# Performance work log

Measured on AMD Instinct MI355X. Metric: run time of the kernel, lower is better.

## Reference

```python
import jax, jax.numpy as jnp
import numpy as np

NEG_SLOPE = 0.01  # torch F.leaky_relu default


def _leaky_relu(v):
    return jnp.where(v >= 0, v, NEG_SLOPE * v)


def _att_layer(t, w1, w2):
    # t: [b, c, n] ; SE-style channel attention with scalar gate
    y = t.mean(axis=-1)                                   # [b, c] (AdaptiveAvgPool1d(1))
    y = jax.nn.sigmoid(jax.nn.relu(y @ w1.T) @ w2.T)       # [b, 1]
    return t * y[:, :, None]


def _avwgcn(x, node_emb, supports, cheb, wpool, bpool, iw, ib, gw, gb,
            a1w1, a1w2, a2w1, a2w2):
    # x: [b, n, c_in]; supports/cheb: [k, n, n]
    b, n, _ = x.shape
    weights = jnp.einsum('nd,dkio->nkio', node_emb, wpool)   # per-node dyn weights
    bias = node_emb @ bpool                                  # [n, o]
    x_g = jnp.einsum('knm,bmc->bnkc', supports, x)           # [b, n, k, c_in]
    x_gconv0 = jnp.einsum('bnki,nkio->bno', x_g, weights) + bias
    x0 = x @ iw.T + ib                                       # init_gconv: [b, n, o]
    x_g1 = jnp.einsum('knm,bmc->bnkc', cheb, x0).reshape(b, n, -1)
    x_gconv1 = x_g1 @ gw.T + gb                              # [b, n, o]
    out = (_att_layer(_leaky_relu(x_gconv0).transpose(0, 2, 1), a1w1, a1w2)
           + _att_layer(_leaky_relu(x_gconv1).transpose(0, 2, 1), a2w1, a2w2))
    return out.transpose(0, 2, 1)                            # [b, n, o]


def _cheb_supports(L, k):
    n = L.shape[0]
    s = [jnp.eye(n, dtype=L.dtype), L]
    for _ in range(2, k):
        s.append(2.0 * L @ s[-1] - s[-2])
    return jnp.stack(s, axis=0)  # [k, n, n]


B, N, DIN, DOUT, K, ED = 64, 1024, 32, 64, 3, 16
CIN = DIN + DOUT  # 96 (gate/update input = cat(x, state))


def setup_inputs() -> dict:
    key = jax.random.key(0)
    ks = jax.random.split(key, 32)
    g = lambda i, shape, s=0.1: jax.random.normal(ks[i], shape, dtype=jnp.float32) * s
    inp = {
        'x': jax.random.normal(ks[0], (B, N, DIN), dtype=jnp.float32),
        'state': jax.random.normal(ks[1], (B, N, DOUT), dtype=jnp.float32),
        'node_embeddings': jax.random.normal(ks[2], (N, ED), dtype=jnp.float32),
        'learned_tilde': jax.random.normal(ks[3], (N, N), dtype=jnp.float32) / np.sqrt(N),
        'cheb_polynomials': jax.random.normal(ks[4], (K, N, N), dtype=jnp.float32) / np.sqrt(N),
        # gate AVWGCN: dim_in=96, dim_out=2*DOUT=128
        'gate_wpool': g(5, (ED, K, CIN, 2 * DOUT)),
        'gate_bpool': g(6, (ED, 2 * DOUT)),
        'gate_iw': g(7, (2 * DOUT, CIN)), 'gate_ib': g(8, (2 * DOUT,)),
        'gate_gw': g(9, (2 * DOUT, 2 * DOUT * K)), 'gate_gb': g(10, (2 * DOUT,)),
        'gate_a1w1': g(11, (2 * DOUT // 16, 2 * DOUT)), 'gate_a1w2': g(12, (1, 2 * DOUT // 16)),
        'gate_a2w1': g(13, (2 * DOUT // 16, 2 * DOUT)), 'gate_a2w2': g(14, (1, 2 * DOUT // 16)),
        # update AVWGCN: dim_in=96, dim_out=DOUT=64
        'upd_wpool': g(15, (ED, K, CIN, DOUT)),
        'upd_bpool': g(16, (ED, DOUT)),
        'upd_iw': g(17, (DOUT, CIN)), 'upd_ib': g(18, (DOUT,)),
        'upd_gw': g(19, (DOUT, DOUT * K)), 'upd_gb': g(20, (DOUT,)),
        'upd_a1w1': g(21, (DOUT // 16, DOUT)), 'upd_a1w2': g(22, (1, DOUT // 16)),
        'upd_a2w1': g(23, (DOUT // 16, DOUT)), 'upd_a2w2': g(24, (1, DOUT // 16)),
    }
    return inp


def reference(x, state, node_embeddings, learned_tilde, cheb_polynomials,
              gate_wpool, gate_bpool, gate_iw, gate_ib, gate_gw, gate_gb,
              gate_a1w1, gate_a1w2, gate_a2w1, gate_a2w2,
              upd_wpool, upd_bpool, upd_iw, upd_ib, upd_gw, upd_gb,
              upd_a1w1, upd_a1w2, upd_a2w1, upd_a2w2):
    supports = _cheb_supports(learned_tilde, K)  # [k, n, n]
    inp_state = jnp.concatenate([x, state], axis=-1)  # [b, n, din+dout]
    z_r = jax.nn.sigmoid(_avwgcn(inp_state, node_embeddings, supports, cheb_polynomials,
                                 gate_wpool, gate_bpool, gate_iw, gate_ib, gate_gw, gate_gb,
                                 gate_a1w1, gate_a1w2, gate_a2w1, gate_a2w2))
    z, r = jnp.split(z_r, 2, axis=-1)
    candidate = jnp.concatenate([x, z * state], axis=-1)
    hc = jnp.tanh(_avwgcn(candidate, node_embeddings, supports, cheb_polynomials,
                          upd_wpool, upd_bpool, upd_iw, upd_ib, upd_gw, upd_gb,
                          upd_a1w1, upd_a1w2, upd_a2w1, upd_a2w2))
    h = r * state + (1.0 - r) * hc
    return h
```

## Files before the change

### kernel.cpp

```cpp
#include <hip/hip_runtime.h>
#include <hip/hip_bf16.h>
#include <math.h>


#define B_  64
#define N_  1024
#define CIN_ 96
#define R_  288

typedef __attribute__((ext_vector_type(8))) short bf16x8;
typedef __attribute__((ext_vector_type(4))) float f32x4;
typedef unsigned short u16;
typedef unsigned int u32;

__device__ __forceinline__ float lrelu(float v) { return v >= 0.f ? v : 0.01f * v; }
__device__ __forceinline__ float sigmoidf_(float u) { return 1.f / (1.f + expf(-u)); }
__device__ __forceinline__ u16 f2b(float f) {
  union { float f; u32 u; } c; c.f = f;
  u32 u = c.u;
  return (u16)((u + 0x7FFFu + ((u >> 16) & 1u)) >> 16);
}
__device__ __forceinline__ float b2f(u16 u) {
  union { u32 x; float f; } c; c.x = ((u32)u) << 16; return c.f;
}
__device__ __forceinline__ void gload_lds16(const u16* gp, u16* lp) {
  __builtin_amdgcn_global_load_lds((const __attribute__((address_space(1))) u32*)gp,
                                   (__attribute__((address_space(3))) u32*)lp, 16, 0, 0);
}

__global__ __launch_bounds__(256) void concat_bf2(const float* __restrict__ x,
                                                  const float* __restrict__ st,
                                                  float* __restrict__ inp,
                                                  u16* __restrict__ inpb) {
  size_t t = (size_t)blockIdx.x * 256 + threadIdx.x;
  if (t >= (size_t)B_ * N_ * CIN_) return;
  int i = (int)(t % CIN_);
  size_t v = t / CIN_;
  size_t b = v & 63, n = v >> 6;
  float f = (i < 32) ? x[(b * N_ + n) * 32 + i] : st[(b * N_ + n) * 64 + (i - 32)];
  inp[t] = f;
  inpb[t] = f2b(f);
}

__global__ __launch_bounds__(256) void conv_f2b(const float* __restrict__ in,
                                                u16* __restrict__ out, int n4) {
  int t = blockIdx.x * 256 + threadIdx.x;
  if (t >= n4) return;
  float4 v = ((const float4*)in)[t];
  ushort4 o;
  o.x = f2b(v.x); o.y = f2b(v.y); o.z = f2b(v.z); o.w = f2b(v.w);
  ((ushort4*)out)[t] = o;
}

__global__ __launch_bounds__(256) void split_hilo(const float* __restrict__ in,
                                                  u16* __restrict__ hi,
                                                  u16* __restrict__ lo, int n4) {
  int t = blockIdx.x * 256 + threadIdx.x;
  if (t >= n4) return;
  float4 v = ((const float4*)in)[t];
  ushort4 h, l;
  h.x = f2b(v.x); l.x = f2b(v.x - b2f(h.x));
  h.y = f2b(v.y); l.y = f2b(v.y - b2f(h.y));
  h.z = f2b(v.z); l.z = f2b(v.z - b2f(h.z));
  h.w = f2b(v.w); l.w = f2b(v.w - b2f(h.w));
  ((ushort4*)hi)[t] = h;
  ((ushort4*)lo)[t] = l;
}

__global__ __launch_bounds__(256) void transpose_split(const float* __restrict__ in,
                                                       u16* __restrict__ hiT,
                                                       u16* __restrict__ loT) {
  __shared__ float t[32][33];
  const int tid = threadIdx.x;
  const int j0 = blockIdx.x * 32, r0 = blockIdx.y * 32;
  const int tc = tid & 31, tr = tid >> 5;
#pragma unroll
  for (int q = 0; q < 4; ++q)
    t[tr + q * 8][tc] = in[(size_t)(r0 + tr + q * 8) * 1024 + j0 + tc];
  __syncthreads();
  const int jj = tid >> 3, rq = (tid & 7) * 4;
  ushort4 h, l;
#pragma unroll
  for (int q = 0; q < 4; ++q) {
    float v = t[rq + q][jj];
    u16 hh = f2b(v);
    ((u16*)&h)[q] = hh;
    ((u16*)&l)[q] = f2b(v - b2f(hh));
  }
  *(ushort4*)(hiT + (size_t)(j0 + jj) * N_ + r0 + rq) = h;
  *(ushort4*)(loT + (size_t)(j0 + jj) * N_ + r0 + rq) = l;
}

__global__ __launch_bounds__(256) void transpose_b2b(const u16* __restrict__ Z, int Zs,
                                                     int Ctot, u16* __restrict__ Zt) {
  __shared__ u16 t[32][36];
  const int tid = threadIdx.x;
  const int c0 = blockIdx.x * 32, n0 = blockIdx.y * 32, b = blockIdx.z;
  {
    const int i = tid >> 3, c4 = (tid & 7) * 4;
    ushort4 v = *(const ushort4*)(Z + ((size_t)(n0 + i) * 64 + b) * Zs + c0 + c4);
    t[i][c4] = v.x; t[i][c4 + 1] = v.y; t[i][c4 + 2] = v.z; t[i][c4 + 3] = v.w;
  }
  __syncthreads();
  {
    const int c = tid >> 3, n4 = (tid & 7) * 4;
    ushort4 o;
    o.x = t[n4][c]; o.y = t[n4 + 1][c]; o.z = t[n4 + 2][c]; o.w = t[n4 + 3][c];
    *(ushort4*)(Zt + (size_t)(b * Ctot + c0 + c) * 1024 + n0 + n4) = o;
  }
}

__global__ __launch_bounds__(256) void mfma_l2p(const u16* __restrict__ Lhi,
                                                const u16* __restrict__ Llo,
                                                const u16* __restrict__ LhiT,
                                                const u16* __restrict__ LloT,
                                                float* __restrict__ P) {
  __shared__ u16 Asl[64 * 64];
  __shared__ u16 Bsl[64 * 64];
  const int tid = threadIdx.x;
  const int w = tid >> 6, lane = tid & 63;
  const int m0 = blockIdx.y * 64, n0 = blockIdx.x * 64;
  const int ph = blockIdx.z;
  const int wr = w >> 1, wc = w & 1;
  const int sr = lane >> 3, so = lane & 7;
  const int cl = lane & 15, q4 = lane >> 4;
  f32x4 acc[2][2] = {};

  const u16* A = (ph == 1) ? Llo : Lhi;
  const u16* B = (ph == 2) ? LloT : LhiT;
  for (int k0 = 0; k0 < 1024; k0 += 64) {
    __syncthreads();
#pragma unroll
    for (int i = 0; i < 2; ++i) {
      const int r = i * 32 + w * 8 + sr;
      const int o = so ^ (r & 7);
      gload_lds16(A + (size_t)(m0 + r) * 1024 + k0 + o * 8, Asl + (i * 32 + w * 8) * 64);
      gload_lds16(B + (size_t)(n0 + r) * 1024 + k0 + o * 8, Bsl + (i * 32 + w * 8) * 64);
    }
    __syncthreads();
#pragma unroll
    for (int kk = 0; kk < 2; ++kk) {
      bf16x8 af[2], bfr[2];
#pragma unroll
      for (int mi = 0; mi < 2; ++mi) {
        const int ra = wr * 32 + mi * 16 + cl;
        af[mi] = *(const bf16x8*)(Asl + ra * 64 + ((kk * 4 + q4) ^ (ra & 7)) * 8);
      }
#pragma unroll
      for (int ni = 0; ni < 2; ++ni) {
        const int rb = wc * 32 + ni * 16 + cl;
        bfr[ni] = *(const bf16x8*)(Bsl + rb * 64 + ((kk * 4 + q4) ^ (rb & 7)) * 8);
      }
#pragma unroll
      for (int mi = 0; mi < 2; ++mi)
#pragma unroll
        for (int ni = 0; ni < 2; ++ni)
          acc[mi][ni] = __builtin_amdgcn_mfma_f32_16x16x32_bf16(af[mi], bfr[ni], acc[mi][ni], 0, 0, 0);
    }
  }
  float* Pz = P + ((size_t)ph << 20);
#pragma unroll
  for (int mi = 0; mi < 2; ++mi)
#pragma unroll
    for (int ni = 0; ni < 2; ++ni) {
      const int j = n0 + wc * 32 + ni * 16 + cl;
#pragma unroll
      for (int r = 0; r < 4; ++r) {
        const int m = m0 + wr * 32 + mi * 16 + q4 * 4 + r;
        Pz[(size_t)m * 1024 + j] = acc[mi][ni][r];
      }
    }
}

__global__ __launch_bounds__(256) void l2_finish(const float* __restrict__ P,
                                                 u16* __restrict__ Y) {
  int t = blockIdx.x * 256 + threadIdx.x;
  float4 a = ((const float4*)P)[t];
  float4 b = ((const float4*)(P + 1048576))[t];
  float4 c = ((const float4*)(P + 2097152))[t];
  int e = t << 2;
  int m = e >> 10, j = e & 1023;
  ushort4 o;
  o.x = f2b(2.f * (a.x + b.x + c.x) - (m == j     ? 1.f : 0.f));
  o.y = f2b(2.f * (a.y + b.y + c.y) - (m == j + 1 ? 1.f : 0.f));
  o.z = f2b(2.f * (a.z + b.z + c.z) - (m == j + 2 ? 1.f : 0.f));
  o.w = f2b(2.f * (a.w + b.w + c.w) - (m == j + 3 ? 1.f : 0.f));
  ((ushort4*)Y)[t] = o;
}

__global__ __launch_bounds__(256) void mfma_stack_f32(const u16* __restrict__ A,
                                                      const u16* __restrict__ Bt,
                                                      float* __restrict__ Y, int J) {
  __shared__ u16 Asl[2][128 * 32];
  __shared__ u16 Bsl[2][128 * 32];
  const int tid = threadIdx.x;
  const int w = tid >> 6, lane = tid & 63;
  const int m0 = blockIdx.y * 128, n0 = blockIdx.x * 128;
  const int wr = w >> 1, wc = w & 1;
  const int sr = lane >> 2, so = lane & 3;
  const int cl = lane & 15, q4 = lane >> 4;
  f32x4 acc[4][4] = {};

  auto STAGE = [&](u16* Ad, u16* Bd, int k0) {
#pragma unroll
    for (int i = 0; i < 2; ++i) {
      const int r = i * 64 + w * 16 + sr;
      const int o = so ^ ((r >> 1) & 3);
      gload_lds16(A + (size_t)(m0 + r) * 1024 + k0 + o * 8, Ad + (i * 64 + w * 16) * 32);
      gload_lds16(Bt + (size_t)(n0 + r) * 1024 + k0 + o * 8, Bd + (i * 64 + w * 16) * 32);
    }
  };
  auto COMPUTE = [&](const u16* As, const u16* Bs) {
    bf16x8 af[4], bfr[4];
#pragma unroll
    for (int mi = 0; mi < 4; ++mi) {
      const int ra = wr * 64 + mi * 16 + cl;
      af[mi] = *(const bf16x8*)(As + ra * 32 + (q4 ^ ((ra >> 1) & 3)) * 8);
    }
#pragma unroll
    for (int ni = 0; ni < 4; ++ni) {
      const int rb = wc * 64 + ni * 16 + cl;
      bfr[ni] = *(const bf16x8*)(Bs + rb * 32 + (q4 ^ ((rb >> 1) & 3)) * 8);
    }
#pragma unroll
    for (int mi = 0; mi < 4; ++mi)
#pragma unroll
      for (int ni = 0; ni < 4; ++ni)
        acc[mi][ni] = __builtin_amdgcn_mfma_f32_16x16x32_bf16(af[mi], bfr[ni], acc[mi][ni], 0, 0, 0);
  };

  STAGE(Asl[0], Bsl[0], 0);
  for (int k0 = 0; k0 < 1024; k0 += 64) {
    STAGE(Asl[1], Bsl[1], k0 + 32);
    asm volatile("s_waitcnt vmcnt(4)" ::: "memory");
    __builtin_amdgcn_s_barrier();
    __builtin_amdgcn_sched_barrier(0);
    COMPUTE(Asl[0], Bsl[0]);
    asm volatile("s_waitcnt lgkmcnt(0)" ::: "memory");
    __builtin_amdgcn_s_barrier();
    __builtin_amdgcn_sched_barrier(0);
    if (k0 + 64 < 1024) {
      STAGE(Asl[0], Bsl[0], k0 + 64);
      asm volatile("s_waitcnt vmcnt(4)" ::: "memory");
    } else {
      asm volatile("s_waitcnt vmcnt(0)" ::: "memory");
    }
    __builtin_amdgcn_s_barrier();
    __builtin_amdgcn_sched_barrier(0);
    COMPUTE(Asl[1], Bsl[1]);
    asm volatile("s_waitcnt lgkmcnt(0)" ::: "memory");
    __builtin_amdgcn_s_barrier();
    __builtin_amdgcn_sched_barrier(0);
  }
#pragma unroll
  for (int mi = 0; mi < 4; ++mi)
#pragma unroll
    for (int ni = 0; ni < 4; ++ni) {
      const int j = n0 + wc * 64 + ni * 16 + cl;
#pragma unroll
      for (int r = 0; r < 4; ++r) {
        const int m = m0 + wr * 64 + mi * 16 + q4 * 4 + r;
        Y[(size_t)m * J + j] = acc[mi][ni][r];
      }
    }
}

template <int O, int OSH>
__global__ __launch_bounds__(128) void vgen2(const float* __restrict__ gw,
                                             const float* __restrict__ iw,
                                             const float* __restrict__ ib,
                                             int Ctot,
                                             u16* __restrict__ Vb,
                                             float* __restrict__ ball) {
  const int c = blockIdx.x;
  const int col = threadIdx.x;
  if (c >= Ctot) {
    if (col < 96) Vb[(size_t)c * 96 + col] = 0;
    else if (col == 96) ball[c] = 0.f;
    return;
  }
  __shared__ float sg[O];
  const int o = c & (O - 1), k = c >> OSH;
  const float* g = gw + (size_t)o * (3 * O) + (size_t)k * O;
  for (int e = col; e < O; e += 128) sg[e] = g[e];
  __syncthreads();
  if (col < 96) {
    float s = 0.f;
#pragma unroll
    for (int j = 0; j < O; ++j) s += sg[j] * iw[j * 96 + col];
    Vb[(size_t)c * 96 + col] = f2b(s);
  } else if (col == 96) {
    float s = 0.f;
#pragma unroll
    for (int j = 0; j < O; ++j) s += sg[j] * ib[j];
    ball[c] = s;
  }
}

__global__ __launch_bounds__(256) void zgemm(const u16* __restrict__ A,
                                             const u16* __restrict__ Bt,
                                             const float* __restrict__ ball,
                                             u16* __restrict__ Z, int Zs) {
  __shared__ u16 Asl[128 * 32];
  __shared__ u16 Bsl[128 * 32];
  const int tid = threadIdx.x;
  const int w = tid >> 6, lane = tid & 63;
  const int m0 = blockIdx.y * 128, n0 = blockIdx.x * 128;
  const int wr = w >> 1, wc = w & 1;
  const int sr = lane >> 2, so = lane & 3;
  const int cl = lane & 15, q4 = lane >> 4;
  f32x4 acc[4][4] = {};
  for (int k0 = 0; k0 < 96; k0 += 32) {
    __syncthreads();
#pragma unroll
    for (int i = 0; i < 2; ++i) {
      const int r = i * 64 + w * 16 + sr;
      const int o = so ^ (r & 3);
      gload_lds16(A + (size_t)(m0 + r) * 96 + k0 + o * 8, Asl + (i * 64 + w * 16) * 32);
      gload_lds16(Bt + (size_t)(n0 + r) * 96 + k0 + o * 8, Bsl + (i * 64 + w * 16) * 32);
    }
    __syncthreads();
    bf16x8 af[4], bfr[4];
#pragma unroll
    for (int mi = 0; mi < 4; ++mi) {
      const int ra = wr * 64 + mi * 16 + cl;
      af[mi] = *(const bf16x8*)(Asl + ra * 32 + (q4 ^ (ra & 3)) * 8);
    }
#pragma unroll
    for (int ni = 0; ni < 4; ++ni) {
      const int rb = wc * 64 + ni * 16 + cl;
      bfr[ni] = *(const bf16x8*)(Bsl + rb * 32 + (q4 ^ (rb & 3)) * 8);
    }
#pragma unroll
    for (int mi = 0; mi < 4; ++mi)
#pragma unroll
      for (int ni = 0; ni < 4; ++ni)
        acc[mi][ni] = __builtin_amdgcn_mfma_f32_16x16x32_bf16(af[mi], bfr[ni], acc[mi][ni], 0, 0, 0);
  }
#pragma unroll
  for (int mi = 0; mi < 4; ++mi)
#pragma unroll
    for (int ni = 0; ni < 4; ++ni) {
      const int c = n0 + wc * 64 + ni * 16 + cl;
      const float bb = ball[c];
#pragma unroll
      for (int r = 0; r < 4; ++r) {
        const int m = m0 + wr * 64 + mi * 16 + q4 * 4 + r;
        Z[(size_t)m * Zs + c] = f2b(acc[mi][ni][r] + bb);
      }
    }
}

__global__ __launch_bounds__(512) void mfma_k3(const u16* __restrict__ A3,
                                               const u16* __restrict__ Zt,
                                               const float* __restrict__ gb,
                                               float* __restrict__ Y,
                                               int J, int obits) {
  __shared__ u16 Asl[2][128 * 64];
  __shared__ u16 Bsl[2][128 * 64];
  const int tid = threadIdx.x;
  const int w = tid >> 6, lane = tid & 63;
  const int m0 = blockIdx.y * 128, n0 = blockIdx.x * 128;
  const int wr = w >> 2, wc = w & 3;
  const int sr = lane >> 3, so = lane & 7;
  const int cl = lane & 15, q4 = lane >> 4;
  const int omask = (1 << obits) - 1;
  f32x4 acc[4][2] = {};

  auto STAGE = [&](u16* Ad, u16* Bd, int k0) {
    const int kb = k0 >> 10, ko = k0 & 1023;
#pragma unroll
    for (int i = 0; i < 2; ++i) {
      const int r = i * 64 + w * 8 + sr;
      const int o = so ^ (r & 7);
      gload_lds16(A3 + (size_t)kb * 1048576 + (size_t)(m0 + r) * 1024 + ko + o * 8,
                  Ad + (i * 64 + w * 8) * 64);
      const int jp = n0 + r;
      const int brow = (((jp >> obits) * 3 + kb) << obits) | (jp & omask);
      gload_lds16(Zt + (size_t)brow * 1024 + ko + o * 8, Bd + (i * 64 + w * 8) * 64);
    }
  };
  auto COMPUTE = [&](const u16* As, const u16* Bs) {
#pragma unroll
    for (int kk = 0; kk < 2; ++kk) {
      bf16x8 af[4], bfr[2];
#pragma unroll
      for (int mi = 0; mi < 4; ++mi) {
        const int ra = wr * 64 + mi * 16 + cl;
        af[mi] = *(const bf16x8*)(As + ra * 64 + ((kk * 4 + q4) ^ (ra & 7)) * 8);
      }
#pragma unroll
      for (int ni = 0; ni < 2; ++ni) {
        const int rb = wc * 32 + ni * 16 + cl;
        bfr[ni] = *(const bf16x8*)(Bs + rb * 64 + ((kk * 4 + q4) ^ (rb & 7)) * 8);
      }
#pragma unroll
      for (int mi = 0; mi < 4; ++mi)
#pragma unroll
        for (int ni = 0; ni < 2; ++ni)
          acc[mi][ni] = __builtin_amdgcn_mfma_f32_16x16x32_bf16(af[mi], bfr[ni], acc[mi][ni], 0, 0, 0);
    }
  };

  STAGE(Asl[0], Bsl[0], 0);
  for (int k0 = 0; k0 < 3072; k0 += 128) {
    STAGE(Asl[1], Bsl[1], k0 + 64);
    asm volatile("s_waitcnt vmcnt(4)" ::: "memory");
    __builtin_amdgcn_s_barrier();
    __builtin_amdgcn_sched_barrier(0);
    COMPUTE(Asl[0], Bsl[0]);
    asm volatile("s_waitcnt lgkmcnt(0)" ::: "memory");
    __builtin_amdgcn_s_barrier();
    __builtin_amdgcn_sched_barrier(0);
    if (k0 + 128 < 3072) {
      STAGE(Asl[0], Bsl[0], k0 + 128);
      asm volatile("s_waitcnt vmcnt(4)" ::: "memory");
    } else {
      asm volatile("s_waitcnt vmcnt(0)" ::: "memory");
    }
    __builtin_amdgcn_s_barrier();
    __builtin_amdgcn_sched_barrier(0);
    COMPUTE(Asl[1], Bsl[1]);
    asm volatile("s_waitcnt lgkmcnt(0)" ::: "memory");
    __builtin_amdgcn_s_barrier();
    __builtin_amdgcn_sched_barrier(0);
  }
#pragma unroll
  for (int mi = 0; mi < 4; ++mi)
#pragma unroll
    for (int ni = 0; ni < 2; ++ni) {
      const int j = n0 + wc * 32 + ni * 16 + cl;
      const float bb = gb[j & omask];
#pragma unroll
      for (int r = 0; r < 4; ++r) {
        const int m = m0 + wr * 64 + mi * 16 + q4 * 4 + r;
        Y[(size_t)m * J + j] = acc[mi][ni][r] + bb;
      }
    }
}

__global__ __launch_bounds__(256) void weightgen3(const float* __restrict__ emb,
                                                  const float* __restrict__ wpool,
                                                  int Otot, int o0, u16* __restrict__ W) {
  const int tid = threadIdx.x;
  const int ro = blockIdx.x * 256 + tid;
  const int r = ro >> 6, o = ro & 63;
  const int n0 = blockIdx.y * 64;
  __shared__ float semb[64][17];
  for (int e = tid; e < 1024; e += 256) semb[e >> 4][e & 15] = emb[(n0 + (e >> 4)) * 16 + (e & 15)];
  __syncthreads();
  float wv[16];
#pragma unroll
  for (int d = 0; d < 16; ++d) wv[d] = wpool[((size_t)d * R_ + r) * Otot + o0 + o];
#pragma unroll 4
  for (int n = 0; n < 64; ++n) {
    float s = 0.f;
#pragma unroll
    for (int d = 0; d < 16; ++d) s += semb[n][d] * wv[d];
    W[(size_t)(n0 + n) * (R_ * 64) + ro] = f2b(s);
  }
}

__global__ __launch_bounds__(256) void pernode5(const float* __restrict__ xa,
                                                const float* __restrict__ xbc,
                                                const u16* __restrict__ W,
                                                const float* __restrict__ emb,
                                                const float* __restrict__ bpool,
                                                int Otot, int o0,
                                                float* __restrict__ outp) {
  const int n = blockIdx.x;
  const int tid = threadIdx.x;
  __shared__ float sW[32][68];
  __shared__ float sX[32][68];
  __shared__ float semb[16];
  if (tid < 16) semb[tid] = emb[n * 16 + tid];
  const int tx = tid & 31, tb = tid >> 5;
  const int lb = tid >> 2, li = (tid & 3) * 8;
  float acc[8][2] = {};
  const u16* Wn = W + (size_t)n * (R_ * 64);

  for (int c = 0; c < 9; ++c) {
    const int k = c / 3, i0 = (c % 3) * 32;
    const float* xk = (k == 0) ? (xa + (size_t)n * 6144)
                               : (xbc + ((size_t)(k - 1) * 1024 + n) * 6144);
    __syncthreads();
    {
      const int row = tid >> 3, o8 = (tid & 7) * 8;
      uint4 v = *(const uint4*)(Wn + (size_t)(c * 32 + row) * 64 + o8);
      sW[row][o8 + 0] = b2f((u16)(v.x & 0xFFFF)); sW[row][o8 + 1] = b2f((u16)(v.x >> 16));
      sW[row][o8 + 2] = b2f((u16)(v.y & 0xFFFF)); sW[row][o8 + 3] = b2f((u16)(v.y >> 16));
      sW[row][o8 + 4] = b2f((u16)(v.z & 0xFFFF)); sW[row][o8 + 5] = b2f((u16)(v.z >> 16));
      sW[row][o8 + 6] = b2f((u16)(v.w & 0xFFFF)); sW[row][o8 + 7] = b2f((u16)(v.w >> 16));
    }
    {
      const float* p = xk + (size_t)lb * 96 + i0 + li;
      float4 v0 = *(const float4*)p;
      float4 v1 = *(const float4*)(p + 4);
      sX[li + 0][lb] = v0.x; sX[li + 1][lb] = v0.y;
      sX[li + 2][lb] = v0.z; sX[li + 3][lb] = v0.w;
      sX[li + 4][lb] = v1.x; sX[li + 5][lb] = v1.y;
      sX[li + 6][lb] = v1.z; sX[li + 7][lb] = v1.w;
    }
    __syncthreads();
#pragma unroll
    for (int il = 0; il < 32; ++il) {
      float xv[8], wv[2];
#pragma unroll
      for (int j = 0; j < 8; ++j) xv[j] = sX[il][tb * 8 + j];
      wv[0] = sW[il][tx * 2]; wv[1] = sW[il][tx * 2 + 1];
#pragma unroll
      for (int j = 0; j < 8; ++j) { acc[j][0] += xv[j] * wv[0]; acc[j][1] += xv[j] * wv[1]; }
    }
  }
  float bias[2];
#pragma unroll
  for (int qq = 0; qq < 2; ++qq) {
    int o = o0 + tx * 2 + qq;
    float s = 0.f;
#pragma unroll
    for (int d = 0; d < 16; ++d) s += semb[d] * bpool[d * Otot + o];
    bias[qq] = s;
  }
#pragma unroll
  for (int j = 0; j < 8; ++j) {
    size_t base = ((size_t)n * B_ + tb * 8 + j) * Otot + o0 + tx * 2;
    outp[base] = acc[j][0] + bias[0];
    outp[base + 1] = acc[j][1] + bias[1];
  }
}

template <int C>
__global__ __launch_bounds__(256) void att_reduce(const float* __restrict__ A0,
                                                  const float* __restrict__ A1,
                                                  float* __restrict__ part0,
                                                  float* __restrict__ part1) {
  constexpr int C4 = C / 4;
  constexpr int H = 256 / C4;
  const int chunk = blockIdx.x;
  const int b = blockIdx.y;
  const int tid = threadIdx.x;
  const int c4 = tid % C4, h = tid / C4;
  __shared__ float4 r0[256], r1[256];
  float4 s0 = {0.f, 0.f, 0.f, 0.f}, s1 = {0.f, 0.f, 0.f, 0.f};
  const float4* p0 = (const float4*)(A0 + (size_t)b * C) + c4;
  const float4* p1 = (const float4*)(A1 + (size_t)b * C) + c4;
  const size_t stride = (size_t)B_ * C4;
  for (int n = chunk * 64 + h; n < chunk * 64 + 64; n += H) {
    float4 v0 = p0[(size_t)n * stride];
    float4 v1 = p1[(size_t)n * stride];
    s0.x += lrelu(v0.x); s0.y += lrelu(v0.y); s0.z += lrelu(v0.z); s0.w += lrelu(v0.w);
    s1.x += lrelu(v1.x); s1.y += lrelu(v1.y); s1.z += lrelu(v1.z); s1.w += lrelu(v1.w);
  }
  r0[tid] = s0; r1[tid] = s1;
  __syncthreads();
  if (h == 0) {
    for (int hh = 1; hh < H; ++hh) {
      float4 a = r0[c4 + hh * C4], bb = r1[c4 + hh * C4];
      s0.x += a.x; s0.y += a.y; s0.z += a.z; s0.w += a.w;
      s1.x += bb.x; s1.y += bb.y; s1.z += bb.z; s1.w += bb.w;
    }
    ((float4*)(part0 + ((size_t)b * 16 + chunk) * C))[c4] = s0;
    ((float4*)(part1 + ((size_t)b * 16 + chunk) * C))[c4] = s1;
  }
}

template <int C, int HID>
__global__ __launch_bounds__(256) void att_finish(const float* __restrict__ part0,
                                                  const float* __restrict__ part1,
                                                  const float* __restrict__ w11,
                                                  const float* __restrict__ w12,
                                                  const float* __restrict__ w21,
                                                  const float* __restrict__ w22,
                                                  float* __restrict__ sout) {
  const int b = blockIdx.x;
  const int tid = threadIdx.x;
  __shared__ float sm0[C], sm1[C];
  __shared__ float h0[HID], h1[HID];
  if (tid < C) {
    float s0 = 0.f, s1 = 0.f;
    for (int ch = 0; ch < 16; ++ch) {
      s0 += part0[((size_t)b * 16 + ch) * C + tid];
      s1 += part1[((size_t)b * 16 + ch) * C + tid];
    }
    sm0[tid] = s0 * (1.f / N_); sm1[tid] = s1 * (1.f / N_);
  }
  __syncthreads();
  if (tid < HID) {
    float a = 0.f;
    for (int cc = 0; cc < C; ++cc) a += sm0[cc] * w11[tid * C + cc];
    h0[tid] = fmaxf(a, 0.f);
  } else if (tid >= 32 && tid < 32 + HID) {
    int j = tid - 32;
    float a = 0.f;
    for (int cc = 0; cc < C; ++cc) a += sm1[cc] * w21[j * C + cc];
    h1[j] = fmaxf(a, 0.f);
  }
  __syncthreads();
  if (tid == 0) {
    float a = 0.f;
    for (int j = 0; j < HID; ++j) a += h0[j] * w12[j];
    sout[b] = sigmoidf_(a);
  } else if (tid == 32) {
    float a = 0.f;
    for (int j = 0; j < HID; ++j) a += h1[j] * w22[j];
    sout[B_ + b] = sigmoidf_(a);
  }
}

__global__ __launch_bounds__(256) void gate_combine_b2(const float* __restrict__ a0,
                                                       const float* __restrict__ a1,
                                                       const float* __restrict__ s12,
                                                       const float* __restrict__ x,
                                                       const float* __restrict__ st,
                                                       float* __restrict__ cand,
                                                       u16* __restrict__ candb,
                                                       float* __restrict__ rbuf) {
  size_t t = (size_t)blockIdx.x * 256 + threadIdx.x;
  if (t >= (size_t)B_ * N_ * 64) return;
  int c = (int)(t & 63);
  int b = (int)((t >> 6) & 63);
  int n = (int)(t >> 12);
  float s1 = s12[b], s2 = s12[B_ + b];
  size_t nb = (size_t)n * B_ + b;
  size_t i128 = nb * 128;
  float uz = s1 * lrelu(a0[i128 + c]) + s2 * lrelu(a1[i128 + c]);
  float ur = s1 * lrelu(a0[i128 + 64 + c]) + s2 * lrelu(a1[i128 + 64 + c]);
  float z = sigmoidf_(uz);
  float r = sigmoidf_(ur);
  float stv = st[((size_t)b * N_ + n) * 64 + c];
  float zs = z * stv;
  cand[nb * CIN_ + 32 + c] = zs;
  candb[nb * CIN_ + 32 + c] = f2b(zs);
  rbuf[nb * 64 + c] = r;
  if (c < 32) {
    float xv = x[((size_t)b * N_ + n) * 32 + c];
    cand[nb * CIN_ + c] = xv;
    candb[nb * CIN_ + c] = f2b(xv);
  }
}

__global__ __launch_bounds__(256) void final_h(const float* __restrict__ a0,
                                               const float* __restrict__ a1,
                                               const float* __restrict__ s12,
                                               const float* __restrict__ rbuf,
                                               const float* __restrict__ st,
                                               float* __restrict__ out) {
  size_t t = (size_t)blockIdx.x * 256 + threadIdx.x;
  if (t >= (size_t)B_ * N_ * 64) return;
  int o = (int)(t & 63);
  int n = (int)((t >> 6) & 1023);
  int b = (int)(t >> 16);
  float s1 = s12[b], s2 = s12[B_ + b];
  size_t nb = ((size_t)n * B_ + b) * 64 + o;
  float u = s1 * lrelu(a0[nb]) + s2 * lrelu(a1[nb]);
  float hc = tanhf(u);
  float r = rbuf[nb];
  out[t] = r * st[t] + (1.f - r) * hc;
}

extern "C" void kernel_launch(void* const* d_in, const int* in_sizes, int n_in,
                              void* d_out, int out_size, void* d_ws, size_t ws_size,
                              hipStream_t stream) {
  const float* x       = (const float*)d_in[0];
  const float* state   = (const float*)d_in[1];
  const float* emb     = (const float*)d_in[2];
  const float* Ltil    = (const float*)d_in[3];
  const float* cheb    = (const float*)d_in[4];
  const float* g_wpool = (const float*)d_in[5];
  const float* g_bpool = (const float*)d_in[6];
  const float* g_iw    = (const float*)d_in[7];
  const float* g_ib    = (const float*)d_in[8];
  const float* g_gw    = (const float*)d_in[9];
  const float* g_gb    = (const float*)d_in[10];
  const float* g_a1w1  = (const float*)d_in[11];
  const float* g_a1w2  = (const float*)d_in[12];
  const float* g_a2w1  = (const float*)d_in[13];
  const float* g_a2w2  = (const float*)d_in[14];
  const float* u_wpool = (const float*)d_in[15];
  const float* u_bpool = (const float*)d_in[16];
  const float* u_iw    = (const float*)d_in[17];
  const float* u_ib    = (const float*)d_in[18];
  const float* u_gw    = (const float*)d_in[19];
  const float* u_gb    = (const float*)d_in[20];
  const float* u_a1w1  = (const float*)d_in[21];
  const float* u_a1w2  = (const float*)d_in[22];
  const float* u_a2w1  = (const float*)d_in[23];
  const float* u_a2w2  = (const float*)d_in[24];
  float* out = (float*)d_out;

  float* ws    = (float*)d_ws;
  float* inp   = ws;
  u16*   inpb  = (u16*)(ws + 6291456);
  float* t12   = ws + 9437184;
  u16*   Zbuf  = (u16*)t12;
  u16*   Wbuf  = (u16*)(ws + 22020096);
  u16*   Btp   = (u16*)(ws + 31457280);
  u16*   Zt    = Wbuf;
  float* acc1  = ws + 34603008;
  float* acc0  = ws + 42991616;
  u16*   LbStk = (u16*)(ws + 51380224);
  u16*   chebb = (u16*)(ws + 52428800);
  float* s12   = ws + 54001664;
  float* s12u  = ws + 54001792;
  float* part0 = ws + 54001920;
  float* part1 = ws + 54132992;
  float* rbuf  = ws + 54264064;
  u16*   Vbg   = (u16*)(ws + 58458368);
  float* bag   = ws + 58476800;
  u16*   Vbu   = (u16*)(ws + 58477184);
  float* bau   = ws + 58489472;
  u16*   LhiT  = (u16*)(ws + 58489728);
  u16*   LloT  = (u16*)(ws + 59014016);
  u16*   Llo   = (u16*)(ws + 59538304);

  dim3 blk(256);
  dim3 blk512(512);

  split_hilo<<<1024, blk, 0, stream>>>(Ltil, LbStk, Llo, 262144);
  transpose_split<<<dim3(32, 32), blk, 0, stream>>>(Ltil, LhiT, LloT);
  mfma_l2p<<<dim3(16, 16, 3), blk, 0, stream>>>(LbStk, Llo, LhiT, LloT, t12);
  l2_finish<<<1024, blk, 0, stream>>>(t12, LbStk + 1048576);
  conv_f2b<<<3072, blk, 0, stream>>>(cheb, chebb, 786432);

  concat_bf2<<<24576, blk, 0, stream>>>(x, state, inp, inpb);
  transpose_b2b<<<dim3(3, 32, 64), blk, 0, stream>>>(inpb, 96, 96, Btp);
  mfma_stack_f32<<<dim3(48, 16), blk, 0, stream>>>(LbStk, Btp, t12, 6144);
  vgen2<128, 7><<<384, dim3(128), 0, stream>>>(g_gw, g_iw, g_ib, 384, Vbg, bag);
  for (int half = 0; half < 2; ++half) {
    weightgen3<<<dim3(72, 16), blk, 0, stream>>>(emb, g_wpool, 128, half * 64, Wbuf);
    pernode5<<<1024, blk, 0, stream>>>(inp, t12, Wbuf, emb, g_bpool, 128, half * 64, acc0);
  }
  zgemm<<<dim3(3, 512), blk, 0, stream>>>(inpb, Vbg, bag, Zbuf, 384);
  transpose_b2b<<<dim3(12, 32, 64), blk, 0, stream>>>(Zbuf, 384, 384, Zt);
  mfma_k3<<<dim3(64, 8), blk512, 0, stream>>>(chebb, Zt, g_gb, acc1, 8192, 7);
  att_reduce<128><<<dim3(16, 64), blk, 0, stream>>>(acc0, acc1, part0, part1);
  att_finish<128, 8><<<64, blk, 0, stream>>>(part0, part1, g_a1w1, g_a1w2, g_a2w1, g_a2w2, s12);
  gate_combine_b2<<<16384, blk, 0, stream>>>(acc0, acc1, s12, x, state, inp, inpb, rbuf);

  transpose_b2b<<<dim3(3, 32, 64), blk, 0, stream>>>(inpb, 96, 96, Btp);
  mfma_stack_f32<<<dim3(48, 16), blk, 0, stream>>>(LbStk, Btp, t12, 6144);
  vgen2<64, 6><<<256, dim3(128), 0, stream>>>(u_gw, u_iw, u_ib, 192, Vbu, bau);
  weightgen3<<<dim3(72, 16), blk, 0, stream>>>(emb, u_wpool, 64, 0, Wbuf);
  pernode5<<<1024, blk, 0, stream>>>(inp, t12, Wbuf, emb, u_bpool, 64, 0, acc0);
  zgemm<<<dim3(2, 512), blk, 0, stream>>>(inpb, Vbu, bau, Zbuf, 256);
  transpose_b2b<<<dim3(6, 32, 64), blk, 0, stream>>>(Zbuf, 256, 192, Zt);
  mfma_k3<<<dim3(32, 8), blk512, 0, stream>>>(chebb, Zt, u_gb, acc1, 4096, 6);
  att_reduce<64><<<dim3(16, 64), blk, 0, stream>>>(acc0, acc1, part0, part1);
  att_finish<64, 4><<<64, blk, 0, stream>>>(part0, part1, u_a1w1, u_a1w2, u_a2w1, u_a2w2, s12u);
  final_h<<<16384, blk, 0, stream>>>(acc0, acc1, s12u, rbuf, state, out);
}
```

Measured before the change: 716.6 us.

## Widen gate per-node conv to 128 outputs and use wider MFMA tile for cheb GEMM

The gate path's per-node weight generation and per-node conv now handle all 128 outputs in one pass instead of two 64-wide halves. This halves the re-reads of the node inputs and the diffusion terms, and removes two launches. The gate cheb GEMM switches to a new kernel with a 128x256 output tile per 512-thread block, so more outputs share each staged A tile. The cost is more accumulator registers, a larger Wbuf footprint (the 128-wide weights) and more LDS per block, which may lower occupancy.

```diff
diff --git a/kernel.cpp b/kernel.cpp
--- a/kernel.cpp
+++ b/kernel.cpp
@@ -439,45 +439,140 @@
     }
 }
 
-__global__ __launch_bounds__(256) void weightgen3(const float* __restrict__ emb,
-                                                  const float* __restrict__ wpool,
-                                                  int Otot, int o0, u16* __restrict__ W) {
+__global__ __launch_bounds__(512) void mfma_k3w(const u16* __restrict__ A3,
+                                                const u16* __restrict__ Zt,
+                                                const float* __restrict__ gb,
+                                                float* __restrict__ Y,
+                                                int J, int obits) {
+  __shared__ u16 Asl[2][128 * 64];
+  __shared__ u16 Bsl[2][256 * 64];
+  const int tid = threadIdx.x;
+  const int w = tid >> 6, lane = tid & 63;
+  const int m0 = blockIdx.y * 128, n0 = blockIdx.x * 256;
+  const int wr = w >> 2, wc = w & 3;
+  const int sr = lane >> 3, so = lane & 7;
+  const int cl = lane & 15, q4 = lane >> 4;
+  const int omask = (1 << obits) - 1;
+  f32x4 acc[4][4] = {};
+
+  auto STAGE = [&](u16* Ad, u16* Bd, int k0) {
+    const int kb = k0 >> 10, ko = k0 & 1023;
+#pragma unroll
+    for (int i = 0; i < 2; ++i) {
+      const int r = i * 64 + w * 8 + sr;
+      const int o = so ^ (r & 7);
+      gload_lds16(A3 + (size_t)kb * 1048576 + (size_t)(m0 + r) * 1024 + ko + o * 8,
+                  Ad + (i * 64 + w * 8) * 64);
+    }
+#pragma unroll
+    for (int i = 0; i < 4; ++i) {
+      const int r = i * 64 + w * 8 + sr;
+      const int o = so ^ (r & 7);
+      const int jp = n0 + r;
+      const int brow = (((jp >> obits) * 3 + kb) << obits) | (jp & omask);
+      gload_lds16(Zt + (size_t)brow * 1024 + ko + o * 8, Bd + (i * 64 + w * 8) * 64);
+    }
+  };
+  auto COMPUTE = [&](const u16* As, const u16* Bs) {
+#pragma unroll
+    for (int kk = 0; kk < 2; ++kk) {
+      bf16x8 af[4], bfr[4];
+#pragma unroll
+      for (int mi = 0; mi < 4; ++mi) {
+        const int ra = wr * 64 + mi * 16 + cl;
+        af[mi] = *(const bf16x8*)(As + ra * 64 + ((kk * 4 + q4) ^ (ra & 7)) * 8);
+      }
+#pragma unroll
+      for (int ni = 0; ni < 4; ++ni) {
+        const int rb = wc * 64 + ni * 16 + cl;
+        bfr[ni] = *(const bf16x8*)(Bs + rb * 64 + ((kk * 4 + q4) ^ (rb & 7)) * 8);
+      }
+#pragma unroll
+      for (int mi = 0; mi < 4; ++mi)
+#pragma unroll
+        for (int ni = 0; ni < 4; ++ni)
+          acc[mi][ni] = __builtin_amdgcn_mfma_f32_16x16x32_bf16(af[mi], bfr[ni], acc[mi][ni], 0, 0, 0);
+    }
+  };
+
+  STAGE(Asl[0], Bsl[0], 0);
+  for (int k0 = 0; k0 < 3072; k0 += 128) {
+    STAGE(Asl[1], Bsl[1], k0 + 64);
+    asm volatile("s_waitcnt vmcnt(6)" ::: "memory");
+    __builtin_amdgcn_s_barrier();
+    __builtin_amdgcn_sched_barrier(0);
+    COMPUTE(Asl[0], Bsl[0]);
+    asm volatile("s_waitcnt lgkmcnt(0)" ::: "memory");
+    __builtin_amdgcn_s_barrier();
+    __builtin_amdgcn_sched_barrier(0);
+    if (k0 + 128 < 3072) {
+      STAGE(Asl[0], Bsl[0], k0 + 128);
+      asm volatile("s_waitcnt vmcnt(6)" ::: "memory");
+    } else {
+      asm volatile("s_waitcnt vmcnt(0)" ::: "memory");
+    }
+    __builtin_amdgcn_s_barrier();
+    __builtin_amdgcn_sched_barrier(0);
+    COMPUTE(Asl[1], Bsl[1]);
+    asm volatile("s_waitcnt lgkmcnt(0)" ::: "memory");
+    __builtin_amdgcn_s_barrier();
+    __builtin_amdgcn_sched_barrier(0);
+  }
+#pragma unroll
+  for (int mi = 0; mi < 4; ++mi)
+#pragma unroll
+    for (int ni = 0; ni < 4; ++ni) {
+      const int j = n0 + wc * 64 + ni * 16 + cl;
+      const float bb = gb[j & omask];
+#pragma unroll
+      for (int r = 0; r < 4; ++r) {
+        const int m = m0 + wr * 64 + mi * 16 + q4 * 4 + r;
+        Y[(size_t)m * J + j] = acc[mi][ni][r] + bb;
+      }
+    }
+}
+
+template <int OW>
+__global__ __launch_bounds__(256) void weightgen3w(const float* __restrict__ emb,
+                                                   const float* __restrict__ wpool,
+                                                   u16* __restrict__ W) {
   const int tid = threadIdx.x;
   const int ro = blockIdx.x * 256 + tid;
-  const int r = ro >> 6, o = ro & 63;
+  const int r = ro / OW, o = ro % OW;
   const int n0 = blockIdx.y * 64;
   __shared__ float semb[64][17];
   for (int e = tid; e < 1024; e += 256) semb[e >> 4][e & 15] = emb[(n0 + (e >> 4)) * 16 + (e & 15)];
   __syncthreads();
   float wv[16];
 #pragma unroll
-  for (int d = 0; d < 16; ++d) wv[d] = wpool[((size_t)d * R_ + r) * Otot + o0 + o];
+  for (int d = 0; d < 16; ++d) wv[d] = wpool[((size_t)d * R_ + r) * OW + o];
 #pragma unroll 4
   for (int n = 0; n < 64; ++n) {
     float s = 0.f;
 #pragma unroll
     for (int d = 0; d < 16; ++d) s += semb[n][d] * wv[d];
-    W[(size_t)(n0 + n) * (R_ * 64) + ro] = f2b(s);
-  }
-}
-
-__global__ __launch_bounds__(256) void pernode5(const float* __restrict__ xa,
+    W[(size_t)(n0 + n) * (R_ * OW) + ro] = f2b(s);
+  }
+}
+
+template <int OW>
+__global__ __launch_bounds__(256) void pernode6(const float* __restrict__ xa,
                                                 const float* __restrict__ xbc,
                                                 const u16* __restrict__ W,
                                                 const float* __restrict__ emb,
                                                 const float* __restrict__ bpool,
-                                                int Otot, int o0,
                                                 float* __restrict__ outp) {
+  constexpr int QO = OW / 32;
   const int n = blockIdx.x;
   const int tid = threadIdx.x;
-  __shared__ float sW[32][68];
+  __shared__ float sW[32][OW + 4];
   __shared__ float sX[32][68];
   __shared__ float semb[16];
   if (tid < 16) semb[tid] = emb[n * 16 + tid];
   const int tx = tid & 31, tb = tid >> 5;
   const int lb = tid >> 2, li = (tid & 3) * 8;
-  float acc[8][2] = {};
-  const u16* Wn = W + (size_t)n * (R_ * 64);
+  float acc[8][QO] = {};
+  const u16* Wn = W + (size_t)n * (R_ * OW);
 
   for (int c = 0; c < 9; ++c) {
     const int k = c / 3, i0 = (c % 3) * 32;
@@ -485,12 +580,16 @@
                                : (xbc + ((size_t)(k - 1) * 1024 + n) * 6144);
     __syncthreads();
     {
-      const int row = tid >> 3, o8 = (tid & 7) * 8;
-      uint4 v = *(const uint4*)(Wn + (size_t)(c * 32 + row) * 64 + o8);
-      sW[row][o8 + 0] = b2f((u16)(v.x & 0xFFFF)); sW[row][o8 + 1] = b2f((u16)(v.x >> 16));
-      sW[row][o8 + 2] = b2f((u16)(v.y & 0xFFFF)); sW[row][o8 + 3] = b2f((u16)(v.y >> 16));
-      sW[row][o8 + 4] = b2f((u16)(v.z & 0xFFFF)); sW[row][o8 + 5] = b2f((u16)(v.z >> 16));
-      sW[row][o8 + 6] = b2f((u16)(v.w & 0xFFFF)); sW[row][o8 + 7] = b2f((u16)(v.w >> 16));
+#pragma unroll
+      for (int it = 0; it < OW / 64; ++it) {
+        const int slot = it * 256 + tid;
+        const int row = slot / (OW / 8), o8 = (slot % (OW / 8)) * 8;
+        uint4 v = *(const uint4*)(Wn + (size_t)(c * 32 + row) * OW + o8);
+        sW[row][o8 + 0] = b2f((u16)(v.x & 0xFFFF)); sW[row][o8 + 1] = b2f((u16)(v.x >> 16));
+        sW[row][o8 + 2] = b2f((u16)(v.y & 0xFFFF)); sW[row][o8 + 3] = b2f((u16)(v.y >> 16));
+        sW[row][o8 + 4] = b2f((u16)(v.z & 0xFFFF)); sW[row][o8 + 5] = b2f((u16)(v.z >> 16));
+        sW[row][o8 + 6] = b2f((u16)(v.w & 0xFFFF)); sW[row][o8 + 7] = b2f((u16)(v.w >> 16));
+      }
     }
     {
       const float* p = xk + (size_t)lb * 96 + i0 + li;
@@ -504,28 +603,31 @@
     __syncthreads();
 #pragma unroll
     for (int il = 0; il < 32; ++il) {
-      float xv[8], wv[2];
+      float xv[8], wv[QO];
 #pragma unroll
       for (int j = 0; j < 8; ++j) xv[j] = sX[il][tb * 8 + j];
-      wv[0] = sW[il][tx * 2]; wv[1] = sW[il][tx * 2 + 1];
-#pragma unroll
-      for (int j = 0; j < 8; ++j) { acc[j][0] += xv[j] * wv[0]; acc[j][1] += xv[j] * wv[1]; }
-    }
-  }
-  float bias[2];
-#pragma unroll
-  for (int qq = 0; qq < 2; ++qq) {
-    int o = o0 + tx * 2 + qq;
+#pragma unroll
+      for (int q = 0; q < QO; ++q) wv[q] = sW[il][tx * QO + q];
+#pragma unroll
+      for (int j = 0; j < 8; ++j)
+#pragma unroll
+        for (int q = 0; q < QO; ++q) acc[j][q] += xv[j] * wv[q];
+    }
+  }
+  float bias[QO];
+#pragma unroll
+  for (int q = 0; q < QO; ++q) {
+    int o = tx * QO + q;
     float s = 0.f;
 #pragma unroll
-    for (int d = 0; d < 16; ++d) s += semb[d] * bpool[d * Otot + o];
-    bias[qq] = s;
+    for (int d = 0; d < 16; ++d) s += semb[d] * bpool[d * OW + o];
+    bias[q] = s;
   }
 #pragma unroll
   for (int j = 0; j < 8; ++j) {
-    size_t base = ((size_t)n * B_ + tb * 8 + j) * Otot + o0 + tx * 2;
-    outp[base] = acc[j][0] + bias[0];
-    outp[base + 1] = acc[j][1] + bias[1];
+    size_t base = ((size_t)n * B_ + tb * 8 + j) * OW + tx * QO;
+#pragma unroll
+    for (int q = 0; q < QO; ++q) outp[base + q] = acc[j][q] + bias[q];
   }
 }
 
@@ -694,6 +796,7 @@
   float* t12   = ws + 9437184;
   u16*   Zbuf  = (u16*)t12;
   u16*   Wbuf  = (u16*)(ws + 22020096);
+  u16*   Wbuf128 = Wbuf;
   u16*   Btp   = (u16*)(ws + 31457280);
   u16*   Zt    = Wbuf;
   float* acc1  = ws + 34603008;
@@ -726,13 +829,11 @@
   transpose_b2b<<<dim3(3, 32, 64), blk, 0, stream>>>(inpb, 96, 96, Btp);
   mfma_stack_f32<<<dim3(48, 16), blk, 0, stream>>>(LbStk, Btp, t12, 6144);
   vgen2<128, 7><<<384, dim3(128), 0, stream>>>(g_gw, g_iw, g_ib, 384, Vbg, bag);
-  for (int half = 0; half < 2; ++half) {
-    weightgen3<<<dim3(72, 16), blk, 0, stream>>>(emb, g_wpool, 128, half * 64, Wbuf);
-    pernode5<<<1024, blk, 0, stream>>>(inp, t12, Wbuf, emb, g_bpool, 128, half * 64, acc0);
-  }
+  weightgen3w<128><<<dim3(144, 16), blk, 0, stream>>>(emb, g_wpool, Wbuf128);
+  pernode6<128><<<1024, blk, 0, stream>>>(inp, t12, Wbuf128, emb, g_bpool, acc0);
   zgemm<<<dim3(3, 512), blk, 0, stream>>>(inpb, Vbg, bag, Zbuf, 384);
   transpose_b2b<<<dim3(12, 32, 64), blk, 0, stream>>>(Zbuf, 384, 384, Zt);
-  mfma_k3<<<dim3(64, 8), blk512, 0, stream>>>(chebb, Zt, g_gb, acc1, 8192, 7);
+  mfma_k3w<<<dim3(32, 8), blk512, 0, stream>>>(chebb, Zt, g_gb, acc1, 8192, 7);
   att_reduce<128><<<dim3(16, 64), blk, 0, stream>>>(acc0, acc1, part0, part1);
   att_finish<128, 8><<<64, blk, 0, stream>>>(part0, part1, g_a1w1, g_a1w2, g_a2w1, g_a2w2, s12);
   gate_combine_b2<<<16384, blk, 0, stream>>>(acc0, acc1, s12, x, state, inp, inpb, rbuf);
@@ -740,8 +841,8 @@
   transpose_b2b<<<dim3(3, 32, 64), blk, 0, stream>>>(inpb, 96, 96, Btp);
   mfma_stack_f32<<<dim3(48, 16), blk, 0, stream>>>(LbStk, Btp, t12, 6144);
   vgen2<64, 6><<<256, dim3(128), 0, stream>>>(u_gw, u_iw, u_ib, 192, Vbu, bau);
-  weightgen3<<<dim3(72, 16), blk, 0, stream>>>(emb, u_wpool, 64, 0, Wbuf);
-  pernode5<<<1024, blk, 0, stream>>>(inp, t12, Wbuf, emb, u_bpool, 64, 0, acc0);
+  weightgen3w<64><<<dim3(72, 16), blk, 0, stream>>>(emb, u_wpool, Wbuf);
+  pernode6<64><<<1024, blk, 0, stream>>>(inp, t12, Wbuf, emb, u_bpool, acc0);
   zgemm<<<dim3(2, 512), blk, 0, stream>>>(inpb, Vbu, bau, Zbuf, 256);
   transpose_b2b<<<dim3(6, 32, 64), blk, 0, stream>>>(Zbuf, 256, 192, Zt);
   mfma_k3<<<dim3(32, 8), blk512, 0, stream>>>(chebb, Zt, u_gb, acc1, 4096, 6);
```

Result: faster. 693.8 us (-3.2%).
